# Performance work log

Hardware: AMD Instinct MI355X
Metric: run time of the kernel (lower is better)

## Reference

```python
import jax, jax.numpy as jnp
import numpy as np


def setup_inputs() -> dict:
    key = jax.random.key(0)
    k1, k2, k3, k4 = jax.random.split(key, 4)
    B, C, Cr, H, W = 4, 32, 16, 64, 128
    return {
        "left_img": jax.random.normal(k1, (B, C, H, W), dtype=jnp.float32),
        "reduce_left_img": jax.random.normal(k2, (B, Cr, H, W), dtype=jnp.float32),
        "right_img": jax.random.normal(k3, (B, C, H, W), dtype=jnp.float32),
        "reduce_right_img": jax.random.normal(k4, (B, Cr, H, W), dtype=jnp.float32),
        "max_disp": 48,
    }


def reference(left_img, reduce_left_img, right_img, reduce_right_img, max_disp):
    # left_img, right_img: [B, C, H, W]; reduce_*: [B, Cr, H, W]
    B, C, H, W = left_img.shape
    D = int(max_disp)
    d = jnp.arange(D)
    cols = jnp.arange(W)
    # valid columns j >= disparity i, zero elsewhere (matches zero_() buffers)
    mask = (cols[None, :] >= d[:, None]).astype(left_img.dtype)  # [D, W]
    mask5 = mask[:, None, :]                                     # [D, 1, W] -> bcast [B,Ch,D,H,W]
    src = jnp.clip(cols[None, :] - d[:, None], 0, W - 1)         # [D, W] shifted source cols

    def shift(x):
        # x: [B, Ch, H, W] -> right-shifted by d with zero fill: [B, Ch, D, H, W]
        y = x[:, :, :, src]              # [B, Ch, H, D, W]
        return jnp.moveaxis(y, 3, 2) * mask5

    l = left_img[:, :, None, :, :] * mask5   # [B, C, D, H, W]
    r = shift(right_img)                     # [B, C, D, H, W]
    ave = (l + r) / 2
    ave2 = (l * l + r * r) / 2
    cost_var = ave2 - ave * ave              # = ((l-r)/2)^2, zero where masked

    cat_l = reduce_left_img[:, :, None, :, :] * mask5  # [B, Cr, D, H, W]
    cat_r = shift(reduce_right_img)                    # [B, Cr, D, H, W]

    # torch: cat((cost_var, cost_cat), 1) with cost_cat = [left_half, right_half]
    return jnp.concatenate([cost_var, cat_l, cat_r], axis=1)
```

## Files before the change

kernel.cpp:

```cpp
#include <hip/hip_runtime.h>

typedef unsigned int u32;
typedef float f32x4 __attribute__((ext_vector_type(4)));

__global__ __launch_bounds__(256) void costvol_kernel(
    const float* __restrict__ left, const float* __restrict__ rleft,
    const float* __restrict__ right, const float* __restrict__ rright,
    float* __restrict__ out)
{
    const u32 bid = blockIdx.x;
    const u32 d = bid % 48u;
    const u32 t = bid / 48u;
    const u32 c = t & 63u;
    const u32 b = t >> 6;
    const u32 tid = threadIdx.x;

    __shared__ float srow[8448];

    float* oplane = out + (size_t)bid * 8192u;

    if (c < 32u) {
        const float* lp = left  + (size_t)(b * 32u + c) * 8192u;
        const float* rp = right + (size_t)(b * 32u + c) * 8192u;

        #pragma unroll
        for (u32 s = 0; s < 8u; ++s) {
            const u32 idx = s * 1024u + tid * 4u;
            const f32x4 v = *(const f32x4*)(rp + idx);
            const u32 sw = idx + (idx >> 5);
            srow[sw]      = v[0];
            srow[sw + 1u] = v[1];
            srow[sw + 2u] = v[2];
            srow[sw + 3u] = v[3];
        }
        __syncthreads();

        #pragma unroll
        for (u32 it = 0; it < 8u; ++it) {
            const u32 flat = it * 1024u + tid * 4u;
            const u32 w0 = flat & 127u;
            const f32x4 l4 = *(const f32x4*)(lp + flat);
            float o[4];
            #pragma unroll
            for (int j = 0; j < 4; ++j) {
                const u32 w = w0 + (u32)j;
                const bool act = (w >= d);
                const u32 ri = act ? (flat + (u32)j - d) : 0u;
                const float r = srow[ri + (ri >> 5)];
                const float tv = (l4[j] - r) * 0.5f;
                o[j] = act ? (tv * tv) : 0.0f;
            }
            f32x4 ov = { o[0], o[1], o[2], o[3] };
            __builtin_nontemporal_store(ov, (f32x4*)(oplane + flat));
        }
    } else if (c < 48u) {
        const float* sp = rleft + (size_t)(b * 16u + (c - 32u)) * 8192u;
        #pragma unroll
        for (u32 it = 0; it < 8u; ++it) {
            const u32 flat = it * 1024u + tid * 4u;
            const u32 w0 = flat & 127u;
            const f32x4 v = *(const f32x4*)(sp + flat);
            f32x4 ov = { (w0      >= d) ? v[0] : 0.0f,
                         (w0 + 1u >= d) ? v[1] : 0.0f,
                         (w0 + 2u >= d) ? v[2] : 0.0f,
                         (w0 + 3u >= d) ? v[3] : 0.0f };
            __builtin_nontemporal_store(ov, (f32x4*)(oplane + flat));
        }
    } else {
        const float* sp = rright + (size_t)(b * 16u + (c - 48u)) * 8192u;

        #pragma unroll
        for (u32 s = 0; s < 8u; ++s) {
            const u32 idx = s * 1024u + tid * 4u;
            const f32x4 v = *(const f32x4*)(sp + idx);
            const u32 sw = idx + (idx >> 5);
            srow[sw]      = v[0];
            srow[sw + 1u] = v[1];
            srow[sw + 2u] = v[2];
            srow[sw + 3u] = v[3];
        }
        __syncthreads();

        #pragma unroll
        for (u32 it = 0; it < 8u; ++it) {
            const u32 flat = it * 1024u + tid * 4u;
            const u32 w0 = flat & 127u;
            float o[4];
            #pragma unroll
            for (int j = 0; j < 4; ++j) {
                const u32 w = w0 + (u32)j;
                const bool act = (w >= d);
                const u32 ri = act ? (flat + (u32)j - d) : 0u;
                o[j] = act ? srow[ri + (ri >> 5)] : 0.0f;
            }
            f32x4 ov = { o[0], o[1], o[2], o[3] };
            __builtin_nontemporal_store(ov, (f32x4*)(oplane + flat));
        }
    }
}

extern "C" void kernel_launch(void* const* d_in, const int* in_sizes, int n_in,
                              void* d_out, int out_size, void* d_ws, size_t ws_size,
                              hipStream_t stream) {
    const float* left   = (const float*)d_in[0];
    const float* rleft  = (const float*)d_in[1];
    const float* right  = (const float*)d_in[2];
    const float* rright = (const float*)d_in[3];
    float* out = (float*)d_out;
    const u32 blocks = 4u * 64u * 48u;
    costvol_kernel<<<blocks, 256, 0, stream>>>(left, rleft, right, rright, out);
}
```

Baseline: 428.1 us.

## Loop disparities inside block to reuse input chunk across all 48 output planes

Reorganizes the grid so each block loads one 8-row chunk of a channel plane once and emits all 48 disparity planes for it, instead of one block per disparity reloading the whole plane. This removes the 48-fold redundant input reads and LDS fills. Nontemporal stores are replaced with regular stores, and the block count drops to 2048, each with a longer serial store loop.

```diff
diff --git a/kernel.cpp b/kernel.cpp
--- a/kernel.cpp
+++ b/kernel.cpp
@@ -9,37 +9,36 @@
     float* __restrict__ out)
 {
     const u32 bid = blockIdx.x;
-    const u32 d = bid % 48u;
-    const u32 t = bid / 48u;
-    const u32 c = t & 63u;
-    const u32 b = t >> 6;
+    const u32 hc = bid & 7u;
+    const u32 t  = bid >> 3;
+    const u32 c  = t & 63u;
+    const u32 b  = t >> 6;
     const u32 tid = threadIdx.x;
 
-    __shared__ float srow[8448];
+    __shared__ float srow[1056];
 
-    float* oplane = out + (size_t)bid * 8192u;
+    const u32 flat = tid * 4u;
+    const u32 w0 = flat & 127u;
+
+    float* obase = out + (size_t)t * 48u * 8192u + hc * 1024u + flat;
 
     if (c < 32u) {
-        const float* lp = left  + (size_t)(b * 32u + c) * 8192u;
-        const float* rp = right + (size_t)(b * 32u + c) * 8192u;
+        const float* lp = left  + (size_t)(b * 32u + c) * 8192u + hc * 1024u;
+        const float* rp = right + (size_t)(b * 32u + c) * 8192u + hc * 1024u;
 
-        #pragma unroll
-        for (u32 s = 0; s < 8u; ++s) {
-            const u32 idx = s * 1024u + tid * 4u;
-            const f32x4 v = *(const f32x4*)(rp + idx);
-            const u32 sw = idx + (idx >> 5);
+        {
+            const f32x4 v = *(const f32x4*)(rp + flat);
+            const u32 sw = flat + (flat >> 5);
             srow[sw]      = v[0];
             srow[sw + 1u] = v[1];
             srow[sw + 2u] = v[2];
             srow[sw + 3u] = v[3];
         }
+        const f32x4 l4 = *(const f32x4*)(lp + flat);
         __syncthreads();
 
-        #pragma unroll
-        for (u32 it = 0; it < 8u; ++it) {
-            const u32 flat = it * 1024u + tid * 4u;
-            const u32 w0 = flat & 127u;
-            const f32x4 l4 = *(const f32x4*)(lp + flat);
+        #pragma unroll 8
+        for (u32 d = 0; d < 48u; ++d) {
             float o[4];
             #pragma unroll
             for (int j = 0; j < 4; ++j) {
@@ -51,29 +50,26 @@
                 o[j] = act ? (tv * tv) : 0.0f;
             }
             f32x4 ov = { o[0], o[1], o[2], o[3] };
-            __builtin_nontemporal_store(ov, (f32x4*)(oplane + flat));
+            *(f32x4*)(obase + d * 8192u) = ov;
         }
     } else if (c < 48u) {
-        const float* sp = rleft + (size_t)(b * 16u + (c - 32u)) * 8192u;
-        #pragma unroll
-        for (u32 it = 0; it < 8u; ++it) {
-            const u32 flat = it * 1024u + tid * 4u;
-            const u32 w0 = flat & 127u;
-            const f32x4 v = *(const f32x4*)(sp + flat);
+        const float* sp = rleft + (size_t)(b * 16u + (c - 32u)) * 8192u + hc * 1024u;
+        const f32x4 v = *(const f32x4*)(sp + flat);
+
+        #pragma unroll 8
+        for (u32 d = 0; d < 48u; ++d) {
             f32x4 ov = { (w0      >= d) ? v[0] : 0.0f,
                          (w0 + 1u >= d) ? v[1] : 0.0f,
                          (w0 + 2u >= d) ? v[2] : 0.0f,
                          (w0 + 3u >= d) ? v[3] : 0.0f };
-            __builtin_nontemporal_store(ov, (f32x4*)(oplane + flat));
+            *(f32x4*)(obase + d * 8192u) = ov;
         }
     } else {
-        const float* sp = rright + (size_t)(b * 16u + (c - 48u)) * 8192u;
+        const float* sp = rright + (size_t)(b * 16u + (c - 48u)) * 8192u + hc * 1024u;
 
-        #pragma unroll
-        for (u32 s = 0; s < 8u; ++s) {
-            const u32 idx = s * 1024u + tid * 4u;
-            const f32x4 v = *(const f32x4*)(sp + idx);
-            const u32 sw = idx + (idx >> 5);
+        {
+            const f32x4 v = *(const f32x4*)(sp + flat);
+            const u32 sw = flat + (flat >> 5);
             srow[sw]      = v[0];
             srow[sw + 1u] = v[1];
             srow[sw + 2u] = v[2];
@@ -81,10 +77,8 @@
         }
         __syncthreads();
 
-        #pragma unroll
-        for (u32 it = 0; it < 8u; ++it) {
-            const u32 flat = it * 1024u + tid * 4u;
-            const u32 w0 = flat & 127u;
+        #pragma unroll 8
+        for (u32 d = 0; d < 48u; ++d) {
             float o[4];
             #pragma unroll
             for (int j = 0; j < 4; ++j) {
@@ -94,7 +88,7 @@
                 o[j] = act ? srow[ri + (ri >> 5)] : 0.0f;
             }
             f32x4 ov = { o[0], o[1], o[2], o[3] };
-            __builtin_nontemporal_store(ov, (f32x4*)(oplane + flat));
+            *(f32x4*)(obase + d * 8192u) = ov;
         }
     }
 }
@@ -107,6 +101,6 @@
     const float* right  = (const float*)d_in[2];
     const float* rright = (const float*)d_in[3];
     float* out = (float*)d_out;
-    const u32 blocks = 4u * 64u * 48u;
+    const u32 blocks = 4u * 64u * 8u;
     costvol_kernel<<<blocks, 256, 0, stream>>>(left, rleft, right, rright, out);
 }
```

New measurement: 401.6 us. -6.2%, faster.
